# Optimization experiments

Hardware: AMD Instinct MI355X
Metric: run time of the kernel (lower is better)

The kernel has to match this reference:

```python
import jax, jax.numpy as jnp
import numpy as np

N_HEADS = 8
HID = 512
HEAD_DIM = HID // N_HEADS
SCALE = float(np.sqrt(HEAD_DIM))  # sqrt(64) = 8


def _heads(x, w, b, n_heads):
    # x: [B,S,D] -> [B,H,S,Dh]
    B, S, D = x.shape
    y = x @ w + b
    return y.reshape(B, S, n_heads, D // n_heads).transpose(0, 2, 1, 3)


def setup_inputs() -> dict:
    key = jax.random.key(0)
    ks = jax.random.split(key, 12)
    B, S, D = 16, 1024, HID
    p = lambda k: jax.random.normal(k, (D, D), jnp.float32) * 0.02
    return {
        "query": jax.random.normal(ks[0], (B, S, D), jnp.float32),
        "key": jax.random.normal(ks[1], (B, S, D), jnp.float32),
        "value": jax.random.normal(ks[2], (B, S, D), jnp.float32),
        "mask": jnp.ones((B, 1, 1, S), jnp.int32),
        "wq": p(ks[3]), "bq": jnp.zeros((D,), jnp.float32),
        "wk": p(ks[4]), "bk": jnp.zeros((D,), jnp.float32),
        "wv": p(ks[5]), "bv": jnp.zeros((D,), jnp.float32),
        "wq1": p(ks[6]), "bq1": jnp.zeros((D,), jnp.float32),
        "wk1": p(ks[7]), "bk1": jnp.zeros((D,), jnp.float32),
        "wfc": p(ks[8]), "bfc": jnp.zeros((D,), jnp.float32),
    }


def reference(query, key, value, mask, wq, bq, wk, bk, wv, bv,
              wq1, bq1, wk1, bk1, wfc, bfc):
    B, S, D = query.shape
    Q = _heads(query, wq, bq, N_HEADS)
    K = _heads(key, wk, bk, N_HEADS)
    V = _heads(value, wv, bv, N_HEADS)
    Q1 = _heads(query, wq1, bq1, N_HEADS)
    K1 = _heads(key, wk1, bk1, N_HEADS)

    energy = jnp.einsum("bhqd,bhkd->bhqk", Q, K) / SCALE
    # eval-mode concrete sample = plain sigmoid of scaled logits
    sample = jax.nn.sigmoid(jnp.einsum("bhqd,bhkd->bhqk", Q1, K1) / SCALE)

    energy = jnp.where(mask == 0, -jnp.inf, energy)
    attention = jax.nn.softmax(energy, axis=-1) * sample

    r_att = jnp.mean(attention, axis=1)  # [B,S,S]
    x = jnp.einsum("bhqk,bhkd->bhqd", attention, V)
    x = x.transpose(0, 2, 1, 3).reshape(B, S, D)
    x = x @ wfc + bfc
    return (x, r_att)
```

## Files before the change

kernel.cpp:

```cpp
#include <hip/hip_runtime.h>
#include <hip/hip_bf16.h>

typedef unsigned short u16;
typedef unsigned int u32;
typedef unsigned long long u64;
typedef __attribute__((ext_vector_type(8))) short short8;
typedef __attribute__((ext_vector_type(4))) float floatx4;

#define MFMA16(a,b,c) __builtin_amdgcn_mfma_f32_16x16x32_bf16((a),(b),(c),0,0,0)

__device__ __forceinline__ u16 f2bf(float f){
  u32 x = __float_as_uint(f);
  x += 0x7FFFu + ((x >> 16) & 1u);
  return (u16)(x >> 16);
}
__device__ __forceinline__ float frcp(float x){ return __builtin_amdgcn_rcpf(x); }
__device__ __forceinline__ float fexp2(float x){ return __builtin_amdgcn_exp2f(x); }
#define KEXP 0.18033688011112042f
#define Z4 ((floatx4){0.f,0.f,0.f,0.f})

__device__ __forceinline__ void gl_lds16(const u16* src, u16* dst){
  __builtin_amdgcn_global_load_lds(
      (const __attribute__((address_space(1))) unsigned int*)(u64)(src),
      (__attribute__((address_space(3))) unsigned int*)(u32)(u64)(dst),
      16, 0, 0);
}

__global__ __launch_bounds__(256) void k_wt6(
    const float* __restrict__ w0, const float* __restrict__ w1, const float* __restrict__ w2,
    const float* __restrict__ w3, const float* __restrict__ w4, const float* __restrict__ w5,
    u16* __restrict__ wts)
{
  int z = blockIdx.y;
  const float* w;
  switch (z){ case 0: w = w0; break; case 1: w = w1; break; case 2: w = w2; break;
              case 3: w = w3; break; case 4: w = w4; break; default: w = w5; break; }
  int idx = blockIdx.x * 256 + threadIdx.x;
  int j = idx >> 9, d = idx & 511;
  wts[(size_t)z * 262144 + idx] = f2bf(w[d * 512 + j]);
}

__global__ __launch_bounds__(256) void k_proj3(
    const float* __restrict__ xq, const float* __restrict__ xk, const float* __restrict__ xv,
    const u16* __restrict__ wts,
    const float* __restrict__ bq, const float* __restrict__ bk, const float* __restrict__ bv,
    const float* __restrict__ bq1, const float* __restrict__ bk1,
    u16* __restrict__ Qh, u16* __restrict__ Kh, u16* __restrict__ Vt,
    u16* __restrict__ Q1h, u16* __restrict__ K1h)
{
  __shared__ __align__(16) u16 As[128][72];
  __shared__ __align__(16) u16 Bs0[128 * 64];
  __shared__ __align__(16) u16 Bs1[128 * 64];
  const int z = blockIdx.z;
  const float* x; const float* bias0; const float* bias1 = nullptr;
  const u16* wtA; const u16* wtB = nullptr;
  u16* out0; u16* out1 = nullptr; int vtm = 0;
  if (z == 0){ x = xq; wtA = wts;                wtB = wts + 3 * 262144;
               bias0 = bq; bias1 = bq1; out0 = Qh; out1 = Q1h; }
  else if (z == 1){ x = xk; wtA = wts + 262144;  wtB = wts + 4 * 262144;
               bias0 = bk; bias1 = bk1; out0 = Kh; out1 = K1h; }
  else { x = xv; wtA = wts + 2 * 262144; bias0 = bv; out0 = Vt; vtm = 1; }

  const int tid = threadIdx.x, lane = tid & 63, wid = tid >> 6;
  const int wm = wid >> 1, wn = wid & 1;
  const int m0 = blockIdx.x * 128, n0 = blockIdx.y * 128;
  const int arow = lane & 15, kg = lane >> 4;
  const int ar = tid >> 1, ah = (tid & 1) * 32;
  const int br = tid >> 3, bc = tid & 7;

  floatx4 acc0[4][4], acc1[4][4];
  #pragma unroll
  for (int i = 0; i < 4; ++i)
    #pragma unroll
    for (int j = 0; j < 4; ++j){ acc0[i][j] = Z4; acc1[i][j] = Z4; }

  for (int k0 = 0; k0 < 512; k0 += 64){
    #pragma unroll
    for (int q = 0; q < 4; ++q)
      gl_lds16(wtA + (size_t)(n0 + q * 32 + br) * 512 + k0 + ((bc ^ (br & 7)) * 8),
               Bs0 + wid * 512 + q * 2048);
    if (z < 2){
      #pragma unroll
      for (int q = 0; q < 4; ++q)
        gl_lds16(wtB + (size_t)(n0 + q * 32 + br) * 512 + k0 + ((bc ^ (br & 7)) * 8),
                 Bs1 + wid * 512 + q * 2048);
    }
    const float4* xp = (const float4*)(x + (size_t)(m0 + ar) * 512 + k0 + ah);
    #pragma unroll
    for (int j = 0; j < 4; ++j){
      float4 f0 = xp[2 * j], f1 = xp[2 * j + 1];
      short8 v;
      v[0] = (short)f2bf(f0.x); v[1] = (short)f2bf(f0.y);
      v[2] = (short)f2bf(f0.z); v[3] = (short)f2bf(f0.w);
      v[4] = (short)f2bf(f1.x); v[5] = (short)f2bf(f1.y);
      v[6] = (short)f2bf(f1.z); v[7] = (short)f2bf(f1.w);
      *(short8*)&As[ar][ah + j * 8] = v;
    }
    __syncthreads();
    #pragma unroll
    for (int kk = 0; kk < 2; ++kk){
      short8 af[4];
      #pragma unroll
      for (int mm = 0; mm < 4; ++mm)
        af[mm] = *(const short8*)&As[wm * 64 + mm * 16 + arow][kk * 32 + kg * 8];
      {
        short8 bf[4];
        #pragma unroll
        for (int nn = 0; nn < 4; ++nn){
          int rr = wn * 64 + nn * 16 + arow;
          bf[nn] = *(const short8*)&Bs0[rr * 64 + ((kk * 32 + kg * 8) ^ ((rr & 7) * 8))];
        }
        #pragma unroll
        for (int mm = 0; mm < 4; ++mm)
          #pragma unroll
          for (int nn = 0; nn < 4; ++nn)
            acc0[mm][nn] = MFMA16(af[mm], bf[nn], acc0[mm][nn]);
      }
      if (z < 2){
        short8 bf[4];
        #pragma unroll
        for (int nn = 0; nn < 4; ++nn){
          int rr = wn * 64 + nn * 16 + arow;
          bf[nn] = *(const short8*)&Bs1[rr * 64 + ((kk * 32 + kg * 8) ^ ((rr & 7) * 8))];
        }
        #pragma unroll
        for (int mm = 0; mm < 4; ++mm)
          #pragma unroll
          for (int nn = 0; nn < 4; ++nn)
            acc1[mm][nn] = MFMA16(af[mm], bf[nn], acc1[mm][nn]);
      }
    }
    __syncthreads();
  }
  #pragma unroll
  for (int mm = 0; mm < 4; ++mm)
    #pragma unroll
    for (int nn = 0; nn < 4; ++nn){
      int j = n0 + wn * 64 + nn * 16 + arow;
      int h = j >> 6, dh = j & 63;
      float b0v = bias0[j];
      #pragma unroll
      for (int i = 0; i < 4; ++i){
        int sg = m0 + wm * 64 + mm * 16 + kg * 4 + i;
        int bb = sg >> 10, s = sg & 1023;
        float val = acc0[mm][nn][i] + b0v;
        size_t o = vtm ? (((size_t)((bb << 3) + h) * 64 + dh) * 1024 + s)
                       : (((size_t)((bb << 3) + h) * 1024 + s) * 64 + dh);
        out0[o] = f2bf(val);
      }
      if (z < 2){
        float b1v = bias1[j];
        #pragma unroll
        for (int i = 0; i < 4; ++i){
          int sg = m0 + wm * 64 + mm * 16 + kg * 4 + i;
          int bb = sg >> 10, s = sg & 1023;
          float val = acc1[mm][nn][i] + b1v;
          out1[(((size_t)((bb << 3) + h) * 1024 + s) * 64 + dh)] = f2bf(val);
        }
      }
    }
}

__global__ void __launch_bounds__(1024)
k_qk(const u16* __restrict__ Qh, const u16* __restrict__ Kh,
     const u16* __restrict__ Q1h, const u16* __restrict__ K1h,
     const int* __restrict__ mask, u16* __restrict__ U, float* __restrict__ rsum)
{
  __shared__ __align__(16) u16 stg[2 * 8192];

  const int tid = threadIdx.x, lane = tid & 63, wid = tid >> 6;
  const int arow = lane & 15, kg = lane >> 4;
  const int b = blockIdx.x, h = blockIdx.y, qs = blockIdx.z;
  const size_t hb = (size_t)(b * 8 + h);

  const int qrow = qs * 256 + wid * 16 + arow;
  const u16* qp  = Qh  + (hb * 1024 + qrow) * 64 + kg * 8;
  const u16* q1p = Q1h + (hb * 1024 + qrow) * 64 + kg * 8;
  short8 aq0 = *(const short8*)qp,  aq1 = *(const short8*)(qp + 32);
  short8 ap0 = *(const short8*)q1p, ap1 = *(const short8*)(q1p + 32);

  u64 mb = 0;
  #pragma unroll
  for (int t = 0; t < 16; ++t)
    #pragma unroll
    for (int cs = 0; cs < 4; ++cs)
      mb |= (mask[b * 1024 + t * 64 + cs * 16 + arow] != 0 ? 1ull : 0ull) << (t * 4 + cs);

  const int ls_half = tid >> 9;
  const int ls_r = (tid & 511) >> 3;
  const int ls_c = (tid & 7) ^ (ls_r & 7);
  u16* const sbase = stg + wid * 512;
  const u16* lsrc = (ls_half ? Kh : K1h) + hb * 65536 + (size_t)ls_r * 64 + ls_c * 8;

  u16* const ubase = U + hb * 1048576;
  const int urow0 = qs * 256 + wid * 16 + kg * 4;

  gl_lds16(lsrc, sbase);
  __syncthreads();

  float sacc[4] = {0.f, 0.f, 0.f, 0.f};
  for (int t = 0; t < 16; ++t){
    if (t < 15)
      gl_lds16(lsrc + (size_t)(t + 1) * 4096, sbase + (((t + 1) & 1) << 13));
    const u16* kb = stg + ((t & 1) << 13);
    #pragma unroll
    for (int cs = 0; cs < 4; ++cs){
      const int krow = cs * 16 + arow;
      const int swl = (krow & 7) * 8;
      short8 b1a = *(const short8*)&kb[krow * 64 + ((     kg * 8) ^ swl)];
      short8 b1b = *(const short8*)&kb[krow * 64 + ((32 + kg * 8) ^ swl)];
      short8 bea = *(const short8*)&kb[4096 + krow * 64 + ((     kg * 8) ^ swl)];
      short8 beb = *(const short8*)&kb[4096 + krow * 64 + ((32 + kg * 8) ^ swl)];
      floatx4 cg4 = Z4, ce4 = Z4;
      cg4 = MFMA16(ap0, b1a, cg4); cg4 = MFMA16(ap1, b1b, cg4);
      ce4 = MFMA16(aq0, bea, ce4); ce4 = MFMA16(aq1, beb, ce4);
      const float msk = ((mb >> (t * 4 + cs)) & 1ull) ? 1.0f : 0.0f;
      #pragma unroll
      for (int i = 0; i < 4; ++i){
        float p = fexp2(ce4[i] * KEXP) * msk;
        float g = frcp(1.0f + fexp2(-cg4[i] * KEXP));
        sacc[i] += p;
        ubase[(size_t)(urow0 + i) * 1024 + t * 64 + cs * 16 + arow] = f2bf(p * g);
      }
    }
    __syncthreads();
  }

  #pragma unroll
  for (int i = 0; i < 4; ++i){
    #pragma unroll
    for (int off = 1; off <= 8; off <<= 1)
      sacc[i] += __shfl_xor(sacc[i], off, 64);
  }
  if (arow == 0){
    #pragma unroll
    for (int i = 0; i < 4; ++i)
      rsum[hb * 1024 + urow0 + i] = sacc[i];
  }
}

__global__ void __launch_bounds__(512)
__attribute__((amdgpu_waves_per_eu(4, 4)))
k_pvr(const u16* __restrict__ U, const float* __restrict__ rsum,
      const u16* __restrict__ Vt, u16* __restrict__ xa, float* __restrict__ ratt)
{
  extern __shared__ __align__(16) u16 stg2[];

  const int tid = threadIdx.x, lane = tid & 63, wid = tid >> 6;
  const int arow = lane & 15, kg = lane >> 4;
  const int b = blockIdx.x, qt = blockIdx.y;
  const int s2 = wid & 1, cg = wid >> 1;
  const int cres = cg * 16 + arow;
  const int wrow = wid * 4;
  const int a_r = s2 * 16 + arow;

  const int ur = tid >> 4, uc = (tid & 15) ^ (ur & 7);
  const int vr0 = tid >> 4, vc0 = (tid & 15) ^ (vr0 & 7);
  const int vr1 = vr0 + 32, vc1 = (tid & 15) ^ (vr1 & 7);

  float racc[4][16];
  #pragma unroll
  for (int r = 0; r < 4; ++r)
    #pragma unroll
    for (int j = 0; j < 16; ++j) racc[r][j] = 0.f;

  for (int h = 0; h < 8; ++h){
    const size_t hb = (size_t)(b * 8 + h);
    const u16* ub = U  + hb * 1048576 + (size_t)(qt * 32) * 1024;
    const u16* vb = Vt + hb * 65536;

    float rlh[4], rlx[4];
    #pragma unroll
    for (int r = 0; r < 4; ++r)
      rlh[r] = frcp(rsum[hb * 1024 + qt * 32 + wrow + r]) * 0.125f;
    #pragma unroll
    for (int i = 0; i < 4; ++i)
      rlx[i] = frcp(rsum[hb * 1024 + qt * 32 + s2 * 16 + kg * 4 + i]);

    gl_lds16(ub + (size_t)ur * 1024 + uc * 8,  stg2 + tid * 8);
    gl_lds16(vb + (size_t)vr0 * 1024 + vc0 * 8, stg2 + 4096 + tid * 8);
    gl_lds16(vb + (size_t)vr1 * 1024 + vc1 * 8, stg2 + 8192 + tid * 8);
    __syncthreads();

    floatx4 cpv = Z4;
    for (int t = 0; t < 8; ++t){
      if (t < 7){
        const int nb = ((t + 1) & 1) * 12288;
        gl_lds16(ub + (size_t)ur * 1024 + (t + 1) * 128 + uc * 8,  stg2 + nb + tid * 8);
        gl_lds16(vb + (size_t)vr0 * 1024 + (t + 1) * 128 + vc0 * 8, stg2 + nb + 4096 + tid * 8);
        gl_lds16(vb + (size_t)vr1 * 1024 + (t + 1) * 128 + vc1 * 8, stg2 + nb + 8192 + tid * 8);
      }
      const u16* Ut  = stg2 + (t & 1) * 12288;
      const u16* Vts = Ut + 4096;
      #pragma unroll
      for (int r = 0; r < 4; ++r){
        const int row = wrow + r;
        u32 w = *(const u32*)&Ut[row * 128 + ((lane * 2) ^ ((row & 7) * 8))];
        racc[r][2 * t]     += __uint_as_float(w << 16) * rlh[r];
        racc[r][2 * t + 1] += __uint_as_float(w & 0xFFFF0000u) * rlh[r];
      }
      #pragma unroll
      for (int ks = 0; ks < 4; ++ks){
        short8 a  = *(const short8*)&Ut[a_r * 128 + ((ks * 32 + kg * 8) ^ ((a_r & 7) * 8))];
        short8 bv = *(const short8*)&Vts[cres * 128 + ((ks * 32 + kg * 8) ^ ((cres & 7) * 8))];
        cpv = MFMA16(a, bv, cpv);
      }
      __syncthreads();
    }
    #pragma unroll
    for (int i = 0; i < 4; ++i){
      const int g = qt * 32 + s2 * 16 + kg * 4 + i;
      xa[((size_t)(b * 1024 + g)) * 512 + h * 64 + cres] = f2bf(cpv[i] * rlx[i]);
    }
  }

  #pragma unroll
  for (int r = 0; r < 4; ++r){
    const size_t rb = ((size_t)(b * 1024 + qt * 32 + wrow + r)) * 1024;
    #pragma unroll
    for (int j = 0; j < 8; ++j){
      float2 v = {racc[r][2 * j], racc[r][2 * j + 1]};
      *(float2*)&ratt[rb + j * 128 + lane * 2] = v;
    }
  }
}

__global__ __launch_bounds__(256) void k_fc(
    const u16* __restrict__ xa, const u16* __restrict__ wt,
    const float* __restrict__ bias, float* __restrict__ out)
{
  __shared__ __align__(16) u16 Asf[128 * 64];
  __shared__ __align__(16) u16 Bsf[128 * 64];
  const int tid = threadIdx.x, lane = tid & 63, wid = tid >> 6;
  const int wm = wid >> 1, wn = wid & 1;
  const int m0 = blockIdx.x * 128, n0 = blockIdx.y * 128;
  const int arow = lane & 15, kg = lane >> 4;
  const int br = tid >> 3, bc = tid & 7;
  u16* const adst = Asf + wid * 512;
  u16* const bdst = Bsf + wid * 512;

  floatx4 acc[4][4];
  #pragma unroll
  for (int i = 0; i < 4; ++i)
    #pragma unroll
    for (int j = 0; j < 4; ++j) acc[i][j] = Z4;

  for (int k0 = 0; k0 < 512; k0 += 64){
    #pragma unroll
    for (int q = 0; q < 4; ++q){
      gl_lds16(xa + (size_t)(m0 + q * 32 + br) * 512 + k0 + ((bc ^ (br & 7)) * 8),
               adst + q * 2048);
      gl_lds16(wt + (size_t)(n0 + q * 32 + br) * 512 + k0 + ((bc ^ (br & 7)) * 8),
               bdst + q * 2048);
    }
    __syncthreads();
    #pragma unroll
    for (int kk = 0; kk < 2; ++kk){
      short8 af[4], bf[4];
      #pragma unroll
      for (int mm = 0; mm < 4; ++mm){
        int rr = wm * 64 + mm * 16 + arow;
        af[mm] = *(const short8*)&Asf[rr * 64 + ((kk * 32 + kg * 8) ^ ((rr & 7) * 8))];
      }
      #pragma unroll
      for (int nn = 0; nn < 4; ++nn){
        int rr = wn * 64 + nn * 16 + arow;
        bf[nn] = *(const short8*)&Bsf[rr * 64 + ((kk * 32 + kg * 8) ^ ((rr & 7) * 8))];
      }
      #pragma unroll
      for (int mm = 0; mm < 4; ++mm)
        #pragma unroll
        for (int nn = 0; nn < 4; ++nn)
          acc[mm][nn] = MFMA16(af[mm], bf[nn], acc[mm][nn]);
    }
    __syncthreads();
  }
  #pragma unroll
  for (int mm = 0; mm < 4; ++mm)
    #pragma unroll
    for (int nn = 0; nn < 4; ++nn){
      int j = n0 + wn * 64 + nn * 16 + arow;
      float bval = bias[j];
      #pragma unroll
      for (int i = 0; i < 4; ++i){
        int sg = m0 + wm * 64 + mm * 16 + kg * 4 + i;
        out[(size_t)sg * 512 + j] = acc[mm][nn][i] + bval;
      }
    }
}

extern "C" void kernel_launch(void* const* d_in, const int* in_sizes, int n_in,
                              void* d_out, int out_size, void* d_ws, size_t ws_size,
                              hipStream_t stream)
{
  const float* query = (const float*)d_in[0];
  const float* key   = (const float*)d_in[1];
  const float* value = (const float*)d_in[2];
  const int*   mask  = (const int*)d_in[3];
  const float* wq  = (const float*)d_in[4];  const float* bq  = (const float*)d_in[5];
  const float* wk  = (const float*)d_in[6];  const float* bk  = (const float*)d_in[7];
  const float* wv  = (const float*)d_in[8];  const float* bv  = (const float*)d_in[9];
  const float* wq1 = (const float*)d_in[10]; const float* bq1 = (const float*)d_in[11];
  const float* wk1 = (const float*)d_in[12]; const float* bk1 = (const float*)d_in[13];
  const float* wfc = (const float*)d_in[14]; const float* bfc = (const float*)d_in[15];

  u16* ws  = (u16*)d_ws;
  u16* Qh  = ws;
  u16* Kh  = Qh  + 8388608;
  u16* Vt  = Kh  + 8388608;
  u16* Q1h = Vt  + 8388608;
  u16* K1h = Q1h + 8388608;
  u16* xa  = K1h + 8388608;
  u16* wts = xa  + 8388608;
  u16* U   = wts + 6 * 262144;
  float* rsum = (float*)(U + 134217728);

  const size_t need_split = (size_t)(51904512 + 134217728) * 2 + 524288;

  float* outx = (float*)d_out;
  float* ratt = outx + 8388608;

  k_wt6<<<dim3(1024, 6), dim3(256), 0, stream>>>(wq, wk, wv, wq1, wk1, wfc, wts);

  k_proj3<<<dim3(128, 4, 3), dim3(256), 0, stream>>>(
      query, key, value, wts, bq, bk, bv, bq1, bk1, Qh, Kh, Vt, Q1h, K1h);

  (void)hipFuncSetAttribute((const void*)k_pvr,
                            hipFuncAttributeMaxDynamicSharedMemorySize, 49152);
  k_qk<<<dim3(16, 8, 4), dim3(1024), 0, stream>>>(
      Qh, Kh, Q1h, K1h, mask, U, rsum);
  k_pvr<<<dim3(16, 32), dim3(512), 49152, stream>>>(
      U, rsum, Vt, xa, ratt);

  k_fc<<<dim3(128, 4), dim3(256), 0, stream>>>(
      xa, wts + 5 * 262144, bfc, outx);
}
```

Baseline: 442.5 us.

## Split fused projection into five independent GEMMs and tile weight transpose via LDS

The weight-transpose kernel now stages 64x64 tiles in shared memory, so global reads and writes are both coalesced instead of doing strided reads. The projection kernel no longer pairs Q/Q1 and K/K1 in one block with two accumulator sets. Instead it launches five grid slices of one GEMM each, balancing work across blocks and halving register and LDS use per block. In exchange, query and key activations are read and converted to bf16 twice.

```diff
diff --git a/kernel.cpp b/kernel.cpp
--- a/kernel.cpp
+++ b/kernel.cpp
@@ -31,16 +31,28 @@
     const float* __restrict__ w3, const float* __restrict__ w4, const float* __restrict__ w5,
     u16* __restrict__ wts)
 {
-  int z = blockIdx.y;
+  __shared__ u16 T[64][66];
+  const int z = blockIdx.z;
   const float* w;
   switch (z){ case 0: w = w0; break; case 1: w = w1; break; case 2: w = w2; break;
               case 3: w = w3; break; case 4: w = w4; break; default: w = w5; break; }
-  int idx = blockIdx.x * 256 + threadIdx.x;
-  int j = idx >> 9, d = idx & 511;
-  wts[(size_t)z * 262144 + idx] = f2bf(w[d * 512 + j]);
-}
-
-__global__ __launch_bounds__(256) void k_proj3(
+  const int j0 = blockIdx.x * 64, d0 = blockIdx.y * 64;
+  const int c = threadIdx.x & 63, r = threadIdx.x >> 6;
+  #pragma unroll
+  for (int it = 0; it < 16; ++it){
+    const int rr = it * 4 + r;
+    T[c][rr] = f2bf(w[(size_t)(d0 + rr) * 512 + j0 + c]);
+  }
+  __syncthreads();
+  u16* out = wts + (size_t)z * 262144;
+  #pragma unroll
+  for (int it = 0; it < 16; ++it){
+    const int jr = it * 4 + r;
+    out[(size_t)(j0 + jr) * 512 + d0 + c] = T[jr][c];
+  }
+}
+
+__global__ __launch_bounds__(256) void k_proj(
     const float* __restrict__ xq, const float* __restrict__ xk, const float* __restrict__ xv,
     const u16* __restrict__ wts,
     const float* __restrict__ bq, const float* __restrict__ bk, const float* __restrict__ bv,
@@ -49,42 +61,36 @@
     u16* __restrict__ Q1h, u16* __restrict__ K1h)
 {
   __shared__ __align__(16) u16 As[128][72];
-  __shared__ __align__(16) u16 Bs0[128 * 64];
-  __shared__ __align__(16) u16 Bs1[128 * 64];
-  const int z = blockIdx.z;
-  const float* x; const float* bias0; const float* bias1 = nullptr;
-  const u16* wtA; const u16* wtB = nullptr;
-  u16* out0; u16* out1 = nullptr; int vtm = 0;
-  if (z == 0){ x = xq; wtA = wts;                wtB = wts + 3 * 262144;
-               bias0 = bq; bias1 = bq1; out0 = Qh; out1 = Q1h; }
-  else if (z == 1){ x = xk; wtA = wts + 262144;  wtB = wts + 4 * 262144;
-               bias0 = bk; bias1 = bk1; out0 = Kh; out1 = K1h; }
-  else { x = xv; wtA = wts + 2 * 262144; bias0 = bv; out0 = Vt; vtm = 1; }
-
+  __shared__ __align__(16) u16 Bs[128 * 64];
+  int z = blockIdx.z;
+  const float* x; const float* bias; u16* out; int vtm = 0;
+  switch (z){
+    case 0: x = xq; bias = bq;  out = Qh;  break;
+    case 1: x = xk; bias = bk;  out = Kh;  break;
+    case 2: x = xv; bias = bv;  out = Vt;  vtm = 1; break;
+    case 3: x = xq; bias = bq1; out = Q1h; break;
+    default: x = xk; bias = bk1; out = K1h; break;
+  }
+  const u16* wt = wts + (size_t)z * 262144;
   const int tid = threadIdx.x, lane = tid & 63, wid = tid >> 6;
   const int wm = wid >> 1, wn = wid & 1;
   const int m0 = blockIdx.x * 128, n0 = blockIdx.y * 128;
   const int arow = lane & 15, kg = lane >> 4;
   const int ar = tid >> 1, ah = (tid & 1) * 32;
   const int br = tid >> 3, bc = tid & 7;
-
-  floatx4 acc0[4][4], acc1[4][4];
+  u16* const bdst = Bs + wid * 512;
+
+  floatx4 acc[4][4];
   #pragma unroll
   for (int i = 0; i < 4; ++i)
     #pragma unroll
-    for (int j = 0; j < 4; ++j){ acc0[i][j] = Z4; acc1[i][j] = Z4; }
+    for (int j = 0; j < 4; ++j) acc[i][j] = Z4;
 
   for (int k0 = 0; k0 < 512; k0 += 64){
     #pragma unroll
     for (int q = 0; q < 4; ++q)
-      gl_lds16(wtA + (size_t)(n0 + q * 32 + br) * 512 + k0 + ((bc ^ (br & 7)) * 8),
-               Bs0 + wid * 512 + q * 2048);
-    if (z < 2){
-      #pragma unroll
-      for (int q = 0; q < 4; ++q)
-        gl_lds16(wtB + (size_t)(n0 + q * 32 + br) * 512 + k0 + ((bc ^ (br & 7)) * 8),
-                 Bs1 + wid * 512 + q * 2048);
-    }
+      gl_lds16(wt + (size_t)(n0 + q * 32 + br) * 512 + k0 + ((bc ^ (br & 7)) * 8),
+               bdst + q * 2048);
     const float4* xp = (const float4*)(x + (size_t)(m0 + ar) * 512 + k0 + ah);
     #pragma unroll
     for (int j = 0; j < 4; ++j){
@@ -99,36 +105,20 @@
     __syncthreads();
     #pragma unroll
     for (int kk = 0; kk < 2; ++kk){
-      short8 af[4];
+      short8 af[4], bf[4];
       #pragma unroll
       for (int mm = 0; mm < 4; ++mm)
         af[mm] = *(const short8*)&As[wm * 64 + mm * 16 + arow][kk * 32 + kg * 8];
-      {
-        short8 bf[4];
+      #pragma unroll
+      for (int nn = 0; nn < 4; ++nn){
+        int rr = wn * 64 + nn * 16 + arow;
+        bf[nn] = *(const short8*)&Bs[rr * 64 + ((kk * 32 + kg * 8) ^ ((rr & 7) * 8))];
+      }
+      #pragma unroll
+      for (int mm = 0; mm < 4; ++mm)
         #pragma unroll
-        for (int nn = 0; nn < 4; ++nn){
-          int rr = wn * 64 + nn * 16 + arow;
-          bf[nn] = *(const short8*)&Bs0[rr * 64 + ((kk * 32 + kg * 8) ^ ((rr & 7) * 8))];
-        }
-        #pragma unroll
-        for (int mm = 0; mm < 4; ++mm)
-          #pragma unroll
-          for (int nn = 0; nn < 4; ++nn)
-            acc0[mm][nn] = MFMA16(af[mm], bf[nn], acc0[mm][nn]);
-      }
-      if (z < 2){
-        short8 bf[4];
-        #pragma unroll
-        for (int nn = 0; nn < 4; ++nn){
-          int rr = wn * 64 + nn * 16 + arow;
-          bf[nn] = *(const short8*)&Bs1[rr * 64 + ((kk * 32 + kg * 8) ^ ((rr & 7) * 8))];
-        }
-        #pragma unroll
-        for (int mm = 0; mm < 4; ++mm)
-          #pragma unroll
-          for (int nn = 0; nn < 4; ++nn)
-            acc1[mm][nn] = MFMA16(af[mm], bf[nn], acc1[mm][nn]);
-      }
+        for (int nn = 0; nn < 4; ++nn)
+          acc[mm][nn] = MFMA16(af[mm], bf[nn], acc[mm][nn]);
     }
     __syncthreads();
   }
@@ -138,25 +128,15 @@
     for (int nn = 0; nn < 4; ++nn){
       int j = n0 + wn * 64 + nn * 16 + arow;
       int h = j >> 6, dh = j & 63;
-      float b0v = bias0[j];
+      float bval = bias[j];
       #pragma unroll
       for (int i = 0; i < 4; ++i){
         int sg = m0 + wm * 64 + mm * 16 + kg * 4 + i;
         int bb = sg >> 10, s = sg & 1023;
-        float val = acc0[mm][nn][i] + b0v;
+        float val = acc[mm][nn][i] + bval;
         size_t o = vtm ? (((size_t)((bb << 3) + h) * 64 + dh) * 1024 + s)
                        : (((size_t)((bb << 3) + h) * 1024 + s) * 64 + dh);
-        out0[o] = f2bf(val);
-      }
-      if (z < 2){
-        float b1v = bias1[j];
-        #pragma unroll
-        for (int i = 0; i < 4; ++i){
-          int sg = m0 + wm * 64 + mm * 16 + kg * 4 + i;
-          int bb = sg >> 10, s = sg & 1023;
-          float val = acc1[mm][nn][i] + b1v;
-          out1[(((size_t)((bb << 3) + h) * 1024 + s) * 64 + dh)] = f2bf(val);
-        }
+        out[o] = f2bf(val);
       }
     }
 }
@@ -415,14 +395,12 @@
   u16* U   = wts + 6 * 262144;
   float* rsum = (float*)(U + 134217728);
 
-  const size_t need_split = (size_t)(51904512 + 134217728) * 2 + 524288;
-
   float* outx = (float*)d_out;
   float* ratt = outx + 8388608;
 
-  k_wt6<<<dim3(1024, 6), dim3(256), 0, stream>>>(wq, wk, wv, wq1, wk1, wfc, wts);
-
-  k_proj3<<<dim3(128, 4, 3), dim3(256), 0, stream>>>(
+  k_wt6<<<dim3(8, 8, 6), dim3(256), 0, stream>>>(wq, wk, wv, wq1, wk1, wfc, wts);
+
+  k_proj<<<dim3(128, 4, 5), dim3(256), 0, stream>>>(
       query, key, value, wts, bq, bk, bv, bq1, bk1, Qh, Kh, Vt, Q1h, K1h);
 
   (void)hipFuncSetAttribute((const void*)k_pvr,
```

Measured after the change: 406.3 us. 8.2% less time.
